# Kernel tuning notes

Measured on AMD Instinct MI355X. Metric: run time of the kernel, lower is better.

The kernel has to match this reference:

```python
import jax, jax.numpy as jnp
import numpy as np

SEARCH = 7
KNN = 7
SIGMA = 1.0
CUTOFF = 1.0
NCLASSES = 20
H, W, N = 64, 2048, 131072


def _inv_gauss_flat(k, sigma):
    # matches get_gaussian_kernel: 2D gaussian on a k x k grid, normalized, then (1 - g)
    ax = np.arange(k, dtype=np.float32)
    xg = np.tile(ax, (k, 1))          # x varies along columns
    yg = xg.T
    mean = (k - 1) / 2.0
    var = sigma ** 2
    g = np.exp(-((xg - mean) ** 2 + (yg - mean) ** 2) / (2.0 * var)) / (2.0 * np.pi * var)
    g = g / g.sum()
    return (1.0 - g).reshape(-1).astype(np.float32)  # [k*k], row-major like F.unfold

_INV_GAUSS = jnp.asarray(_inv_gauss_flat(SEARCH, SIGMA))


def setup_inputs() -> dict:
    key = jax.random.key(0)
    k1, k2, k3, k4, k5 = jax.random.split(key, 5)
    proj_range = jax.random.normal(k1, (H, W), dtype=jnp.float32)  # negatives exercise the <0 -> inf path
    unproj_range = jax.random.uniform(k2, (N,), dtype=jnp.float32)
    proj_argmax = jax.random.randint(k3, (H, W), 0, NCLASSES)
    px = jax.random.randint(k4, (N,), 0, W)
    py = jax.random.randint(k5, (N,), 0, H)
    return {"proj_range": proj_range, "unproj_range": unproj_range,
            "proj_argmax": proj_argmax, "px": px, "py": py}


def reference(proj_range, unproj_range, proj_argmax, px, py):
    pad = (SEARCH - 1) // 2
    S2 = SEARCH * SEARCH
    # F.unfold flattens the kernel row-major: index i -> (dy, dx) = (i // S, i % S)
    dy = jnp.repeat(jnp.arange(SEARCH) - pad, SEARCH)   # [S2]
    dx = jnp.tile(jnp.arange(SEARCH) - pad, SEARCH)     # [S2]

    rows = py[:, None] + dy[None, :]                    # [N, S2]; zero-padded in H
    cols = (px[:, None] + dx[None, :]) % W              # circular padding in W
    valid = (rows >= 0) & (rows < H)
    rows_c = jnp.clip(rows, 0, H - 1)

    nb_range = jnp.where(valid, proj_range[rows_c, cols], 0.0)        # zero pad like F.unfold
    nb_range = jnp.where(nb_range < 0, jnp.inf, nb_range)
    center = (S2 - 1) // 2
    nb_range = nb_range.at[:, center].set(unproj_range)

    k2d = jnp.abs(nb_range - unproj_range[:, None]) * _INV_GAUSS[None, :]  # [N, S2]
    neg_vals, knn_idx = jax.lax.top_k(-k2d, KNN)        # k smallest distances
    knn_dist = -neg_vals                                # == gather(k2d, knn_idx)

    nb_arg = jnp.where(valid, proj_argmax[rows_c, cols], 0)            # zero pad -> class 0
    knn_arg = jnp.take_along_axis(nb_arg, knn_idx, axis=1)             # [N, KNN]
    if CUTOFF > 0:
        knn_arg = jnp.where(knn_dist > CUTOFF, NCLASSES, knn_arg)

    votes = jax.nn.one_hot(knn_arg, NCLASSES + 1, dtype=proj_range.dtype).sum(axis=1)  # [N, C+1]
    knn_out = jnp.argmax(votes[:, 1:-1], axis=1) + 1    # torch: votes[:, 1:-1].argmax + 1
    return knn_out
```

## Files before the change

### kernel.cpp

```cpp
#include <hip/hip_runtime.h>
#include <math.h>

#define SEARCH 7
#define PAD 3
#define S2 49
#define KNN 7
#define NCLASSES 20
#define H 64
#define W 2048
#define NPTS 131072
#define NTILES 32
#define TROWS 70
#define TCOLS 70
#define SPT 32
#define SLICE (NPTS / SPT)
#define KBLOCK 256
#define PPB 128
#define QCAP 512

#define SENTINEL_BITS 0x7FE0000000000000ull
#define CUTOFF_KEYMAX 0x4000000FE000003Full

struct InvG { float v[S2]; };

#define INSF(KEY) do {                                                  \
    double _x = (KEY);                                                  \
    double _t;                                                          \
    _t = fmin(s0, _x); _x = fmax(s0, _x); s0 = _t;                      \
    _t = fmin(s1, _x); _x = fmax(s1, _x); s1 = _t;                      \
    _t = fmin(s2, _x); _x = fmax(s2, _x); s2 = _t;                      \
    _t = fmin(s3, _x); _x = fmax(s3, _x); s3 = _t;                      \
    _t = fmin(s4, _x); _x = fmax(s4, _x); s4 = _t;                      \
    _t = fmin(s5, _x); _x = fmax(s5, _x); s5 = _t;                      \
    s6 = fmin(s6, _x);                                                  \
} while (0)

#define CAND(J, RB, DX) do {                                            \
    float nb = ftile[(RB) + (DX)];                                      \
    nb = (nb < 0.0f) ? __builtin_inff() : nb;                           \
    float d = fabsf(nb - u) * invg.v[J];                                \
    unsigned long long kb = (1ull << 62)                                \
        | ((unsigned long long)__float_as_uint(d) << 6)                 \
        | (unsigned)(J);                                                \
    INSF(__longlong_as_double((long long)kb));                          \
} while (0)

__global__ __launch_bounds__(KBLOCK, 4) void knn_kernel(
    const float* __restrict__ proj_range,
    const float* __restrict__ unproj_range,
    const int* __restrict__ proj_argmax,
    const int* __restrict__ pxv,
    const int* __restrict__ pyv,
    int* __restrict__ outv,
    InvG invg)
{
    __shared__ float         ftile[TROWS * TCOLS];
    __shared__ unsigned char atile[TROWS * TCOLS];
    __shared__ double        kbuf[PPB][KNN];
    __shared__ unsigned queue[QCAP];
    __shared__ int qcnt;

    const int tid  = threadIdx.x;
    const int t    = blockIdx.x >> 5;
    const int sub  = blockIdx.x & 31;
    const int tbase = t << 6;
    const int lane = tid & 63;
    const int wave = tid >> 6;

    if (tid == 0) qcnt = 0;

#pragma unroll
    for (int it = 0; it < 18; ++it) {
        int r = it * 4 + wave;
        if (r < TROWS) {
            int sr = r - 3;
            bool vr = (unsigned)sr < (unsigned)H;
            int gb = (vr ? sr : 0) * W;
            int ca = (tbase - 3 + lane) & (W - 1);
            float fv = proj_range[gb + ca];
            int   av = proj_argmax[gb + ca];
            ftile[r * TCOLS + lane] = vr ? fv : 0.0f;
            atile[r * TCOLS + lane] = (unsigned char)(vr ? av : 0);
            if (lane < TCOLS - 64) {
                int cb = (tbase - 3 + 64 + lane) & (W - 1);
                float fv2 = proj_range[gb + cb];
                int   av2 = proj_argmax[gb + cb];
                ftile[r * TCOLS + 64 + lane] = vr ? fv2 : 0.0f;
                atile[r * TCOLS + 64 + lane] = (unsigned char)(vr ? av2 : 0);
            }
        }
    }
    __syncthreads();

    {
        const int4* px4 = (const int4*)pxv;
        int base4 = (sub * SLICE) >> 2;
#pragma unroll
        for (int k = 0; k < 4; ++k) {
            int idx4 = base4 + k * KBLOCK + tid;
            int4 v = px4[idx4];
            int i0x = idx4 * 4;
#pragma unroll
            for (int e = 0; e < 4; ++e) {
                int x = (e == 0) ? v.x : (e == 1) ? v.y : (e == 2) ? v.z : v.w;
                if ((x >> 6) == t) {
                    int i = i0x + e;
                    int y = pyv[i];
                    int pos = atomicAdd(&qcnt, 1);
                    if (pos < QCAP)
                        queue[pos] = (unsigned)i | ((unsigned)(x & 63) << 17)
                                                | ((unsigned)y << 23);
                }
            }
        }
    }
    __syncthreads();
    const int count = min(qcnt, QCAP);

    const int pairp = wave >> 1;
    const int role  = wave & 1;
    const int pidx  = pairp * 64 + lane;

    for (int base = 0; base < count; base += PPB) {
        int slot = base + pidx;
        bool active = slot < count;
        bool anyact = __ballot(active) != 0;
        unsigned pk = 0u; int i = 0, xl = 0, y = 0;

        if (anyact) {
            pk = active ? queue[slot] : 0u;
            i  = (int)(pk & 0x1FFFFu);
            xl = (int)((pk >> 17) & 63u);
            y  = (int)((pk >> 23) & 63u);
            float u = unproj_range[i];

            double s0, s1, s2, s3, s4, s5, s6;
            s0 = s1 = s2 = s3 = s4 = s5 = s6 =
                __longlong_as_double((long long)SENTINEL_BITS);

            if (role == 0) {
#pragma unroll
                for (int dy = -3; dy <= 0; ++dy) {
                    int rb = (y + dy + 3) * TCOLS + xl + 3;
                    const int dxmax = (dy == 0) ? -1 : 3;
#pragma unroll
                    for (int dx = -3; dx <= dxmax; ++dx) {
                        const int j = (dy + 3) * 7 + (dx + 3);
                        CAND(j, rb, dx);
                    }
                }
            } else {
                INSF(__longlong_as_double((long long)((1ull << 62) | 24ull)));
#pragma unroll
                for (int dy = 0; dy <= 3; ++dy) {
                    int rb = (y + dy + 3) * TCOLS + xl + 3;
                    const int dxmin = (dy == 0) ? 1 : -3;
#pragma unroll
                    for (int dx = dxmin; dx <= 3; ++dx) {
                        const int j = (dy + 3) * 7 + (dx + 3);
                        CAND(j, rb, dx);
                    }
                }
                kbuf[pidx][0] = s0; kbuf[pidx][1] = s1; kbuf[pidx][2] = s2;
                kbuf[pidx][3] = s3; kbuf[pidx][4] = s4; kbuf[pidx][5] = s5;
                kbuf[pidx][6] = s6;
            }
            if (role == 0) {
                __syncthreads();
                double m0 = fmin(s0, kbuf[pidx][6]);
                double m1 = fmin(s1, kbuf[pidx][5]);
                double m2 = fmin(s2, kbuf[pidx][4]);
                double m3 = fmin(s3, kbuf[pidx][3]);
                double m4 = fmin(s4, kbuf[pidx][2]);
                double m5 = fmin(s5, kbuf[pidx][1]);
                double m6 = fmin(s6, kbuf[pidx][0]);

                const double cutmax = __longlong_as_double((long long)CUTOFF_KEYMAX);
                int c0, c1, c2, c3, c4, c5, c6;
#define CLSK(MK, CK) do {                                                \
                long long kb = __double_as_longlong(MK);                 \
                int j = (int)(kb & 63);                                  \
                bool sel = (MK) <= cutmax;                               \
                int dy7 = (j * 37) >> 8;                                 \
                int cc = (int)atile[(y + dy7) * TCOLS + xl + (j - dy7 * 7)]; \
                CK = sel ? cc : 0;                                       \
            } while (0)
                CLSK(m0, c0); CLSK(m1, c1); CLSK(m2, c2); CLSK(m3, c3);
                CLSK(m4, c4); CLSK(m5, c5); CLSK(m6, c6);
#undef CLSK

                int n0 = 1, n1 = 1, n2 = 1, n3 = 1, n4 = 1, n5 = 1, n6 = 1;
#define PAIRV(A, B) do { bool e = (c##A == c##B); n##A += e ? 1 : 0; n##B += e ? 1 : 0; } while (0)
                PAIRV(0,1); PAIRV(0,2); PAIRV(0,3); PAIRV(0,4); PAIRV(0,5); PAIRV(0,6);
                PAIRV(1,2); PAIRV(1,3); PAIRV(1,4); PAIRV(1,5); PAIRV(1,6);
                PAIRV(2,3); PAIRV(2,4); PAIRV(2,5); PAIRV(2,6);
                PAIRV(3,4); PAIRV(3,5); PAIRV(3,6);
                PAIRV(4,5); PAIRV(4,6);
                PAIRV(5,6);
#undef PAIRV

                int best = 0;
#define SCORE(K) do {                                                    \
                bool valid = (unsigned)(c##K - 1) < (unsigned)(NCLASSES - 1);\
                int sc = valid ? ((n##K << 5) | (31 - c##K)) : 0;        \
                best = max(best, sc);                                    \
            } while (0)
                SCORE(0); SCORE(1); SCORE(2); SCORE(3); SCORE(4); SCORE(5); SCORE(6);
#undef SCORE
                if (active) outv[i] = (best == 0) ? 1 : (31 - (best & 31));
                __syncthreads();
            } else {
                __syncthreads();
                __syncthreads();
            }
        } else {
            __syncthreads();
            __syncthreads();
        }
    }
}

extern "C" void kernel_launch(void* const* d_in, const int* in_sizes, int n_in,
                              void* d_out, int out_size, void* d_ws, size_t ws_size,
                              hipStream_t stream) {
    const float* proj_range   = (const float*)d_in[0];
    const float* unproj_range = (const float*)d_in[1];
    const int*   proj_argmax  = (const int*)d_in[2];
    const int*   px           = (const int*)d_in[3];
    const int*   py           = (const int*)d_in[4];
    int* out = (int*)d_out;

    InvG invg;
    float g[S2];
    for (int yy = 0; yy < SEARCH; ++yy) {
        for (int xx = 0; xx < SEARCH; ++xx) {
            float fdx = (float)xx - 3.0f;
            float fdy = (float)yy - 3.0f;
            float s   = fdx * fdx + fdy * fdy;
            float arg = -s / 2.0f;
            float e   = (float)exp((double)arg);
            float gg  = e / 6.2831855f;
            g[yy * SEARCH + xx] = gg;
        }
    }
    float r[8];
    for (int tt = 0; tt < 8; ++tt) r[tt] = g[tt];
    int ii;
    for (ii = 8; ii + 8 <= 48; ii += 8)
        for (int tt = 0; tt < 8; ++tt) r[tt] += g[ii + tt];
    float ssum = ((r[0] + r[1]) + (r[2] + r[3])) + ((r[4] + r[5]) + (r[6] + r[7]));
    for (; ii < S2; ++ii) ssum += g[ii];
    for (int tt = 0; tt < S2; ++tt) invg.v[tt] = 1.0f - (g[tt] / ssum);

    knn_kernel<<<NTILES * SPT, KBLOCK, 0, stream>>>(
        proj_range, unproj_range, proj_argmax, px, py, out, invg);
}
```

Baseline: 21.06 us.

## Halve tile width to double block count and aggregate queue atomics per wave

Each block now covers a 32-column tile instead of 64, so the grid doubles and the shared-memory footprint shrinks. The launch bound is raised to allow more resident blocks. The halo tile is loaded with a flat per-thread index, and per-point LDS atomics are replaced with wave-level ballot/popcount aggregation. The cost is more total halo loading, each px slice being scanned by twice as many blocks, and roughly half as many points per block, which leaves part of the 128-point processing batch idle. The queue overflow guard is also removed and relies on a smaller cap being large enough.

```diff
diff --git a/kernel.cpp b/kernel.cpp
--- a/kernel.cpp
+++ b/kernel.cpp
@@ -9,14 +9,15 @@
 #define H 64
 #define W 2048
 #define NPTS 131072
-#define NTILES 32
+#define NTILES2 64
+#define TILEW 32
 #define TROWS 70
-#define TCOLS 70
+#define TCOLS 38
 #define SPT 32
 #define SLICE (NPTS / SPT)
 #define KBLOCK 256
 #define PPB 128
-#define QCAP 512
+#define QCAP 256
 
 #define SENTINEL_BITS 0x7FE0000000000000ull
 #define CUTOFF_KEYMAX 0x4000000FE000003Full
@@ -45,7 +46,7 @@
     INSF(__longlong_as_double((long long)kb));                          \
 } while (0)
 
-__global__ __launch_bounds__(KBLOCK, 4) void knn_kernel(
+__global__ __launch_bounds__(KBLOCK, 7) void knn_kernel(
     const float* __restrict__ proj_range,
     const float* __restrict__ unproj_range,
     const int* __restrict__ proj_argmax,
@@ -63,38 +64,33 @@
     const int tid  = threadIdx.x;
     const int t    = blockIdx.x >> 5;
     const int sub  = blockIdx.x & 31;
-    const int tbase = t << 6;
+    const int tbase = t << 5;
     const int lane = tid & 63;
     const int wave = tid >> 6;
 
     if (tid == 0) qcnt = 0;
-
-#pragma unroll
-    for (int it = 0; it < 18; ++it) {
-        int r = it * 4 + wave;
-        if (r < TROWS) {
+    __syncthreads();
+
+#pragma unroll
+    for (int it = 0; it < 11; ++it) {
+        int idx = it * KBLOCK + tid;
+        if (idx < TROWS * TCOLS) {
+            int r = (unsigned)idx / TCOLS;
+            int c = idx - r * TCOLS;
             int sr = r - 3;
             bool vr = (unsigned)sr < (unsigned)H;
             int gb = (vr ? sr : 0) * W;
-            int ca = (tbase - 3 + lane) & (W - 1);
+            int ca = (tbase - 3 + c) & (W - 1);
             float fv = proj_range[gb + ca];
             int   av = proj_argmax[gb + ca];
-            ftile[r * TCOLS + lane] = vr ? fv : 0.0f;
-            atile[r * TCOLS + lane] = (unsigned char)(vr ? av : 0);
-            if (lane < TCOLS - 64) {
-                int cb = (tbase - 3 + 64 + lane) & (W - 1);
-                float fv2 = proj_range[gb + cb];
-                int   av2 = proj_argmax[gb + cb];
-                ftile[r * TCOLS + 64 + lane] = vr ? fv2 : 0.0f;
-                atile[r * TCOLS + 64 + lane] = (unsigned char)(vr ? av2 : 0);
-            }
-        }
-    }
-    __syncthreads();
+            ftile[idx] = vr ? fv : 0.0f;
+            atile[idx] = (unsigned char)(vr ? av : 0);
+        }
+    }
 
     {
         const int4* px4 = (const int4*)pxv;
-        int base4 = (sub * SLICE) >> 2;
+        int base4 = sub * (SLICE / 4);
 #pragma unroll
         for (int k = 0; k < 4; ++k) {
             int idx4 = base4 + k * KBLOCK + tid;
@@ -103,13 +99,20 @@
 #pragma unroll
             for (int e = 0; e < 4; ++e) {
                 int x = (e == 0) ? v.x : (e == 1) ? v.y : (e == 2) ? v.z : v.w;
-                if ((x >> 6) == t) {
-                    int i = i0x + e;
-                    int y = pyv[i];
-                    int pos = atomicAdd(&qcnt, 1);
-                    if (pos < QCAP)
-                        queue[pos] = (unsigned)i | ((unsigned)(x & 63) << 17)
-                                                | ((unsigned)y << 23);
+                bool match = (x >> 5) == t;
+                unsigned long long m = __ballot(match);
+                if (m != 0ull) {
+                    int tot = __popcll(m);
+                    int pre = __popcll(m & ((1ull << lane) - 1ull));
+                    int wb = 0;
+                    if (lane == 0) wb = atomicAdd(&qcnt, tot);
+                    wb = __shfl(wb, 0);
+                    if (match) {
+                        int i = i0x + e;
+                        int y = pyv[i];
+                        queue[wb + pre] = (unsigned)i | ((unsigned)(x & 31) << 17)
+                                                     | ((unsigned)y << 22);
+                    }
                 }
             }
         }
@@ -130,8 +133,8 @@
         if (anyact) {
             pk = active ? queue[slot] : 0u;
             i  = (int)(pk & 0x1FFFFu);
-            xl = (int)((pk >> 17) & 63u);
-            y  = (int)((pk >> 23) & 63u);
+            xl = (int)((pk >> 17) & 31u);
+            y  = (int)((pk >> 22) & 63u);
             float u = unproj_range[i];
 
             double s0, s1, s2, s3, s4, s5, s6;
@@ -252,6 +255,6 @@
     for (; ii < S2; ++ii) ssum += g[ii];
     for (int tt = 0; tt < S2; ++tt) invg.v[tt] = 1.0f - (g[tt] / ssum);
 
-    knn_kernel<<<NTILES * SPT, KBLOCK, 0, stream>>>(
+    knn_kernel<<<NTILES2 * SPT, KBLOCK, 0, stream>>>(
         proj_range, unproj_range, proj_argmax, px, py, out, invg);
 }
```

After: 24.78 us. 17.6% more time.
